# Kernel optimization log

Hardware: AMD Instinct MI355X
Metric: run time of the kernel (lower is better)

Reference implementation:

```python
import jax, jax.numpy as jnp
import numpy as np

# ---- layer config (yolov3, layer_no=2) ----
STRIDE = 8
N_CLASSES = 80
IGNORE_TH = 0.7
ANCHORS_PX = np.array([[10,13],[16,30],[33,23],[30,61],[62,45],[59,119],[116,90],[156,198],[373,326]], np.float32)
ALL_ANCHORS = ANCHORS_PX / STRIDE          # [9,2] in grid units
ANCHOR_ID_LO, ANCHOR_ID_HI = 0, 2          # anchor_mask[2] = [0,1,2]
ANCHORS = ALL_ANCHORS[ANCHOR_ID_LO:ANCHOR_ID_HI+1]  # [3,2]
NA = 3
NC = N_CLASSES + 5

B, IN_CH, NG, NBOX = 16, 256, 76, 50


def _safe_log(p):
    # emulate torch BCE's log clamp at -100; eps stops 0*inf -> nan
    return jnp.maximum(jnp.log(jnp.maximum(p, 1e-12)), -100.0)


def _bce_sum(p, t, w=None):
    l = -(t * _safe_log(p) + (1.0 - t) * _safe_log(1.0 - p))
    if w is not None:
        l = l * w
    return l.sum()


def setup_inputs() -> dict:
    key = jax.random.key(0)
    k1, k2, k3, k4, k5 = jax.random.split(key, 5)
    xin = jax.random.normal(k1, (B, IN_CH, NG, NG), jnp.float32)
    cls = jax.random.randint(k2, (B, NBOX, 1), 0, N_CLASSES).astype(jnp.float32)
    cxy = jax.random.uniform(k3, (B, NBOX, 2), jnp.float32, 0.02, 0.98)
    wh = jax.random.uniform(k4, (B, NBOX, 2), jnp.float32, 0.02, 0.40)
    labels = jnp.concatenate([cls, cxy, wh], axis=-1)  # [B,N,5]
    W = jax.random.normal(k5, (NA * NC, IN_CH), jnp.float32) * 0.02  # 1x1 conv
    b = jnp.zeros((NA * NC,), jnp.float32)
    return {"xin": xin, "labels": labels, "W": W, "b": b}


def _yolo_loss(xin, labels, W, b):
    nB, _, nG, _ = xin.shape
    anchors = jnp.asarray(ANCHORS, xin.dtype)          # [3,2]
    all_anchors = jnp.asarray(ALL_ANCHORS, xin.dtype)  # [9,2]

    # 1x1 conv -> [B, A, G, G, C]
    x = jnp.einsum('bchw,oc->bohw', xin, W) + b[None, :, None, None]
    x = x.reshape(nB, NA, NC, nG, nG).transpose(0, 1, 3, 4, 2)

    xy = jax.nn.sigmoid(x[..., :2])
    wh = x[..., 2:4]
    conf_cls = jax.nn.sigmoid(x[..., 4:])  # [B,A,G,G,1+ncls]

    gy, gx = jnp.meshgrid(jnp.arange(nG, dtype=x.dtype), jnp.arange(nG, dtype=x.dtype), indexing='ij')
    pred_boxes = jnp.stack([
        xy[..., 0] + gx,
        xy[..., 1] + gy,
        jnp.exp(wh[..., 0]) * anchors[:, 0][None, :, None, None],
        jnp.exp(wh[..., 1]) * anchors[:, 1][None, :, None, None]], axis=-1)  # [B,A,G,G,4]

    # ---- ground truth ----
    valid = labels.sum(-1) > 0                     # [B,N]
    gt_cls = labels[..., 0].astype(jnp.int32)
    gt = labels[..., 1:] * nG                      # [B,N,4] cx,cy,w,h in grid units
    gt_x, gt_y, gt_w, gt_h = gt[..., 0], gt[..., 1], gt[..., 2], gt[..., 3]
    gi = jnp.floor(gt_x).astype(jnp.int32)
    gj = jnp.floor(gt_y).astype(jnp.int32)

    # best anchor per gt: wh-IoU vs all 9 anchors (centered at origin)
    inter_a = jnp.minimum(gt_w[..., None], all_anchors[:, 0]) * jnp.minimum(gt_h[..., None], all_anchors[:, 1])
    union_a = gt_w[..., None] * gt_h[..., None] + all_anchors[:, 0] * all_anchors[:, 1] - inter_a
    best = jnp.argmax(inter_a / union_a, axis=-1)  # [B,N]
    in_mask = (best >= ANCHOR_ID_LO) & (best <= ANCHOR_ID_HI)
    a = jnp.where(in_mask, best % 3, -1)           # [B,N]

    # all-pairs IoU: pred boxes vs gt boxes (ignore mask)
    pb = pred_boxes.reshape(nB, -1, 4)             # [B,M,4], M = A*G*G
    pa_area = pb[..., 2] * pb[..., 3]
    gt_area = gt_w * gt_h
    tl = jnp.maximum(pb[:, :, None, :2] - pb[:, :, None, 2:] / 2, gt[:, None, :, :2] - gt[:, None, :, 2:] / 2)
    br = jnp.minimum(pb[:, :, None, :2] + pb[:, :, None, 2:] / 2, gt[:, None, :, :2] + gt[:, None, :, 2:] / 2)
    inter = jnp.prod(br - tl, -1) * jnp.all(tl < br, -1)
    iou = inter / (pa_area[:, :, None] + gt_area[:, None, :] - inter)
    iou = jnp.where(valid[:, None, :], iou, 0.0)
    best_iou = iou.max(-1)                         # [B,M]
    has_boxes = valid.any(-1)
    obj_mask = jnp.where(has_boxes[:, None], best_iou <= IGNORE_TH, True).reshape(nB, NA, nG, nG)

    # ---- scatter target assignment ----
    assign = valid & (a >= 0)
    a_safe = jnp.clip(a, 0, NA - 1)
    aw = anchors[a_safe, 0]
    ah = anchors[a_safe, 1]
    tvec = jnp.concatenate([
        (gt_x - jnp.floor(gt_x))[..., None],
        (gt_y - jnp.floor(gt_y))[..., None],
        jnp.log(gt_w / aw + 1e-16)[..., None],
        jnp.log(gt_h / ah + 1e-16)[..., None],
        jnp.ones_like(gt_x)[..., None],
        jax.nn.one_hot(gt_cls, N_CLASSES, dtype=x.dtype)], axis=-1)  # [B,N,NC]
    sval = 2.0 - gt_w * gt_h / (nG * nG)

    bf = jnp.broadcast_to(jnp.arange(nB)[:, None], a.shape).reshape(-1)
    af = jnp.where(assign, a_safe, NA).reshape(-1)  # NA is OOB -> dropped
    jf = gj.reshape(-1)
    if_ = gi.reshape(-1)

    target = jnp.zeros((nB, NA, nG, nG, NC), x.dtype).at[bf, af, jf, if_].set(tvec.reshape(-1, NC), mode='drop')
    scale = jnp.zeros((nB, NA, nG, nG), x.dtype).at[bf, af, jf, if_].set(sval.reshape(-1), mode='drop')
    obj_mask = obj_mask.at[bf, af, jf, if_].set(True, mode='drop')
    noobj = jnp.zeros((nB, NA, nG, nG), bool).at[bf, af, jf, if_].set(True, mode='drop')

    # ---- losses ----
    nm = noobj.astype(x.dtype)[..., None]
    p_obj = conf_cls[..., 0] * obj_mask
    t_obj = target[..., 4] * obj_mask
    p_xy = xy * nm
    t_xy = target[..., :2] * nm
    p_wh = wh * nm
    t_wh = target[..., 2:4] * nm
    p_cls = conf_cls[..., 1:] * nm
    t_cls = target[..., 5:] * nm
    sc = scale[..., None]

    loss_xy = _bce_sum(p_xy, t_xy, sc)
    rs = jnp.sqrt(sc)
    loss_wh = 0.5 * jnp.sum((p_wh * rs - t_wh * rs) ** 2)
    loss_obj = _bce_sum(p_obj, t_obj)
    loss_cls = _bce_sum(p_cls, t_cls)
    loss = loss_xy + loss_wh + loss_obj + loss_cls
    return jnp.stack([loss, loss_xy, loss_wh, loss_obj, loss_cls])


def reference(xin, labels, W, b):
    return _yolo_loss(xin, labels, W, b)
```

## Files before the change

kernel.cpp:

```cpp
#include <hip/hip_runtime.h>
#include <math.h>

#define NB    16
#define NAg   3
#define NCg   85
#define NCLS  80
#define NGg   76
#define NSp   (NGg*NGg)
#define NCELL (NAg*NSp)
#define NBOX  50
#define INCH  256

#define ACC_OFF  0
#define WIN_OFF  32
#define GD_OFF   (WIN_OFF + NB*NCELL*4)
#define GI_OFF   (GD_OFF + NB*NBOX*10*4)
#define PART_OFF (GI_OFF + NB*NBOX*2*4)
#define PART_SZ1 ((size_t)NB*15*NSp*4)
#define NEED4    (PART_OFF + 4*PART_SZ1)
#define NEED1    (PART_OFF + 1*PART_SZ1)
#define ZERO_BYTES GD_OFF

__device__ __constant__ float c_AW[9] = {1.25f,2.0f,4.125f,3.75f,7.75f,7.375f,14.5f,19.5f,46.625f};
__device__ __constant__ float c_AH[9] = {1.625f,3.75f,2.875f,7.625f,5.625f,14.875f,11.25f,24.75f,40.75f};

__device__ __forceinline__ float safe_log(float p) {
    return fmaxf(logf(fmaxf(p, 1e-12f)), -100.0f);
}
__device__ __forceinline__ float sigm(float x) {
    return 1.0f / (1.0f + expf(-x));
}

template<int NSLICE>
__global__ __launch_bounds__(256) void k_gemm_part(
    const float* __restrict__ xin, const float* __restrict__ W,
    float* __restrict__ part)
{
    constexpr int CPS = INCH / NSLICE;
    const int g  = blockIdx.x * 256 + threadIdx.x;
    if (g >= NSp/4) return;
    const int b  = blockIdx.y;
    const int sl = blockIdx.z;
    const int s0 = g * 4;

    float4 acc[15];
#pragma unroll
    for (int f = 0; f < 15; f++) acc[f] = make_float4(0.f,0.f,0.f,0.f);

    const float* xp = xin + ((size_t)b * INCH + sl * CPS) * NSp + s0;
    const float* wp = W + sl * CPS;
#pragma unroll 8
    for (int c = 0; c < CPS; c++) {
        const float4 v = *(const float4*)(xp + (size_t)c * NSp);
#pragma unroll
        for (int f = 0; f < 15; f++) {
            const int row = (f / 5) * NCg + (f % 5);
            const float w = wp[row * INCH + c];
            acc[f].x += w * v.x; acc[f].y += w * v.y;
            acc[f].z += w * v.z; acc[f].w += w * v.w;
        }
    }
#pragma unroll
    for (int f = 0; f < 15; f++)
        *(float4*)&part[(((size_t)sl * NB + b) * 15 + f) * NSp + s0] = acc[f];
}

__global__ void k_labels(const float* __restrict__ labels,
                         float* __restrict__ gdata, int* __restrict__ gint,
                         int* __restrict__ win)
{
    int t = blockIdx.x * blockDim.x + threadIdx.x;
    if (t >= NB * NBOX) return;
    int b = t / NBOX, n = t % NBOX;

    const float* L = labels + (size_t)t * 5;
    float l0 = L[0], l1 = L[1], l2 = L[2], l3 = L[3], l4 = L[4];
    int valid = (l0 + l1 + l2 + l3 + l4) > 0.f;

    float gx = l1 * NGg, gy = l2 * NGg, gw = l3 * NGg, gh = l4 * NGg;

    int best = 0; float brr = -1.f;
#pragma unroll
    for (int k = 0; k < 9; k++) {
        float inter = fminf(gw, c_AW[k]) * fminf(gh, c_AH[k]);
        float uni   = gw*gh + c_AW[k]*c_AH[k] - inter;
        float r     = inter / uni;
        if (r > brr) { brr = r; best = k; }
    }
    int a = (best <= 2) ? best : -1;
    int assign = valid && (a >= 0);
    int a_safe = a < 0 ? 0 : (a > 2 ? 2 : a);

    float* gd = gdata + (size_t)t * 10;
    gd[0] = gx; gd[1] = gy; gd[2] = gw; gd[3] = gh;
    gd[4] = gx - floorf(gx);
    gd[5] = gy - floorf(gy);
    gd[6] = logf(gw / c_AW[a_safe] + 1e-16f);
    gd[7] = logf(gh / c_AH[a_safe] + 1e-16f);
    gd[8] = 2.f - gw * gh / (float)NSp;
    gd[9] = valid ? 1.f : 0.f;

    int gi = (int)floorf(gx), gj = (int)floorf(gy);
    int inb = (gi >= 0) && (gi < NGg) && (gj >= 0) && (gj < NGg);
    int cell = (assign && inb) ? (a * NSp + gj * NGg + gi) : -1;
    gint[t*2 + 0] = cell;
    gint[t*2 + 1] = (int)l0;

    if (cell >= 0) atomicMax(&win[b * NCELL + cell], n + 1);
}

template<int NSLICE>
__global__ __launch_bounds__(256) void k_fuse(
    const float* __restrict__ part, const float* __restrict__ bias,
    const float* __restrict__ gdata, const int* __restrict__ win,
    float* __restrict__ acc)
{
    __shared__ float sb[NBOX][5];
    __shared__ int sHas;
    __shared__ float red[256];

    const int b = blockIdx.y;
    const int tid = threadIdx.x;

    if (tid < NBOX) {
        const float* gd = gdata + ((size_t)b * NBOX + tid) * 10;
        sb[tid][0] = gd[0]; sb[tid][1] = gd[1];
        sb[tid][2] = gd[2]; sb[tid][3] = gd[3];
        sb[tid][4] = gd[9];
    }
    if (tid == 0) sHas = 0;
    __syncthreads();
    if (tid < NBOX && sb[tid][4] > 0.f) atomicOr(&sHas, 1);
    __syncthreads();

    const int cell = blockIdx.x * 256 + tid;
    float l = 0.f;
    if (cell < NCELL) {
        const int a = cell / NSp, s = cell % NSp;
        float x0 = 0.f, x1 = 0.f, x2 = 0.f, x3 = 0.f, x4 = 0.f;
#pragma unroll
        for (int sl = 0; sl < NSLICE; sl++) {
            const float* pp = part + (((size_t)sl * NB + b) * 15 + a * 5) * NSp + s;
            x0 += pp[0*NSp]; x1 += pp[1*NSp]; x2 += pp[2*NSp];
            x3 += pp[3*NSp]; x4 += pp[4*NSp];
        }
        const float gxf = (float)(s % NGg);
        const float gyf = (float)(s / NGg);
        float px = sigm(x0 + bias[a*NCg+0]) + gxf;
        float py = sigm(x1 + bias[a*NCg+1]) + gyf;
        float pw = expf(x2 + bias[a*NCg+2]) * c_AW[a];
        float ph = expf(x3 + bias[a*NCg+3]) * c_AH[a];
        float cf = sigm(x4 + bias[a*NCg+4]);
        float pa = pw * ph;
        float bi = 0.f;
        for (int n = 0; n < NBOX; n++) {
            if (sb[n][4] > 0.f) {
                float gx = sb[n][0], gy = sb[n][1], gw = sb[n][2], gh = sb[n][3];
                float tlx = fmaxf(px - pw*0.5f, gx - gw*0.5f);
                float tly = fmaxf(py - ph*0.5f, gy - gh*0.5f);
                float brx = fminf(px + pw*0.5f, gx + gw*0.5f);
                float bry = fminf(py + ph*0.5f, gy + gh*0.5f);
                float inter = ((tlx < brx) && (tly < bry)) ? (brx-tlx)*(bry-tly) : 0.f;
                float iou = inter / (pa + gw*gh - inter);
                bi = fmaxf(bi, iou);
            }
        }
        bool maskpre  = sHas ? (bi <= 0.7f) : true;
        bool assigned = win[b * NCELL + cell] > 0;
        if (maskpre || assigned) {
            float t = assigned ? 1.f : 0.f;
            l = -(t * safe_log(cf) + (1.f - t) * safe_log(1.f - cf));
        }
    }
    red[tid] = l;
    __syncthreads();
    for (int o = 128; o > 0; o >>= 1) {
        if (tid < o) red[tid] += red[tid + o];
        __syncthreads();
    }
    if (tid == 0) atomicAdd(&acc[2], red[0]);
}

__global__ __launch_bounds__(256) void k_assigned(
    const float* __restrict__ xin, const float* __restrict__ W,
    const float* __restrict__ bias, const float* __restrict__ gdata,
    const int* __restrict__ gint, const int* __restrict__ win,
    float* __restrict__ acc)
{
    const int t = blockIdx.x;
    const int b = t / NBOX, n = t % NBOX;
    const int cell = gint[t*2];
    if (cell < 0) return;
    if (win[b * NCELL + cell] != n + 1) return;

    const int a = cell / NSp, s = cell % NSp;
    const int o0 = a * NCg;
    const int tid = threadIdx.x;

    __shared__ float4 col4[64];
    __shared__ float  xsh[NCg];
    __shared__ float  sacc[3];

    ((float*)col4)[tid] = xin[((size_t)b * INCH + tid) * NSp + s];
    if (tid < 3) sacc[tid] = 0.f;
    __syncthreads();

    const int wid = tid >> 6, lane = tid & 63;
    for (int o = wid; o < NCg; o += 4) {
        const float4 wv = *(const float4*)&W[(size_t)(o0 + o) * INCH + lane * 4];
        const float4 cv = col4[lane];
        float p = wv.x*cv.x + wv.y*cv.y + wv.z*cv.z + wv.w*cv.w;
        for (int off = 32; off; off >>= 1) p += __shfl_down(p, off);
        if (lane == 0) xsh[o] = p + bias[o0 + o];
    }
    __syncthreads();

    if (tid < NCg) {
        const float* gd = gdata + (size_t)t * 10;
        const float sval = gd[8];
        const int gcls = gint[t*2 + 1];
        float val = xsh[tid];
        float term; int slot;
        if (tid < 2) {
            float tgt = gd[4 + tid];
            float p = sigm(val);
            term = -(tgt * safe_log(p) + (1.f - tgt) * safe_log(1.f - p)) * sval;
            slot = 0;
        } else if (tid < 4) {
            float tgt = gd[4 + tid];
            float d = val - tgt;
            term = 0.5f * sval * d * d;
            slot = 1;
        } else if (tid == 4) {
            term = 0.f; slot = 2;
        } else {
            float tgt = ((tid - 5) == gcls) ? 1.f : 0.f;
            float p = sigm(val);
            term = -(tgt * safe_log(p) + (1.f - tgt) * safe_log(1.f - p));
            slot = 2;
        }
        atomicAdd(&sacc[slot], term);
    }
    __syncthreads();
    if (tid == 0) {
        atomicAdd(&acc[0], sacc[0]);
        atomicAdd(&acc[1], sacc[1]);
        atomicAdd(&acc[3], sacc[2]);
    }
}

__global__ void k_final(const float* __restrict__ acc, float* __restrict__ out)
{
    float xy = acc[0], wh = acc[1], ob = acc[2], cl = acc[3];
    out[0] = xy + wh + ob + cl;
    out[1] = xy; out[2] = wh; out[3] = ob; out[4] = cl;
}

extern "C" void kernel_launch(void* const* d_in, const int* in_sizes, int n_in,
                              void* d_out, int out_size, void* d_ws, size_t ws_size,
                              hipStream_t stream)
{
    const float* xin    = (const float*)d_in[0];
    const float* labels = (const float*)d_in[1];
    const float* W      = (const float*)d_in[2];
    const float* bias   = (const float*)d_in[3];

    char* ws = (char*)d_ws;
    float* acc   = (float*)(ws + ACC_OFF);
    int*   win   = (int*)  (ws + WIN_OFF);
    float* gdata = (float*)(ws + GD_OFF);
    int*   gint  = (int*)  (ws + GI_OFF);
    float* part  = (float*)(ws + PART_OFF);
    float* out   = (float*)d_out;

    const bool big = (ws_size >= (size_t)NEED4);

    hipMemsetAsync(ws, 0, ZERO_BYTES, stream);

    k_labels<<<dim3((NB*NBOX + 255)/256), 256, 0, stream>>>(labels, gdata, gint, win);

    const int gx = (NSp/4 + 255) / 256;
    if (big) k_gemm_part<4><<<dim3(gx, NB, 4), 256, 0, stream>>>(xin, W, part);
    else     k_gemm_part<1><<<dim3(gx, NB, 1), 256, 0, stream>>>(xin, W, part);

    const int fx = (NCELL + 255) / 256;
    if (big) k_fuse<4><<<dim3(fx, NB), 256, 0, stream>>>(part, bias, gdata, win, acc);
    else     k_fuse<1><<<dim3(fx, NB), 256, 0, stream>>>(part, bias, gdata, win, acc);

    k_assigned<<<dim3(NB*NBOX), 256, 0, stream>>>(xin, W, bias, gdata, gint, win, acc);
    k_final<<<1, 1, 0, stream>>>(acc, out);
}
```

Before: 203.3 us.

## Fuse partial 1x1-conv GEMM with objectness loss using in-block channel split

```diff
diff --git a/kernel.cpp b/kernel.cpp
--- a/kernel.cpp
+++ b/kernel.cpp
@@ -7,22 +7,21 @@
 #define NCLS  80
 #define NGg   76
 #define NSp   (NGg*NGg)
+#define NG4   (NSp/4)
 #define NCELL (NAg*NSp)
 #define NBOX  50
 #define INCH  256
+#define NTILE 23
 
 #define ACC_OFF  0
 #define WIN_OFF  32
 #define GD_OFF   (WIN_OFF + NB*NCELL*4)
 #define GI_OFF   (GD_OFF + NB*NBOX*10*4)
-#define PART_OFF (GI_OFF + NB*NBOX*2*4)
-#define PART_SZ1 ((size_t)NB*15*NSp*4)
-#define NEED4    (PART_OFF + 4*PART_SZ1)
-#define NEED1    (PART_OFF + 1*PART_SZ1)
 #define ZERO_BYTES GD_OFF
 
 __device__ __constant__ float c_AW[9] = {1.25f,2.0f,4.125f,3.75f,7.75f,7.375f,14.5f,19.5f,46.625f};
 __device__ __constant__ float c_AH[9] = {1.625f,3.75f,2.875f,7.625f,5.625f,14.875f,11.25f,24.75f,40.75f};
+__device__ __constant__ int   c_ROW[15] = {0,1,2,3,4, 85,86,87,88,89, 170,171,172,173,174};
 
 __device__ __forceinline__ float safe_log(float p) {
     return fmaxf(logf(fmaxf(p, 1e-12f)), -100.0f);
@@ -31,38 +30,118 @@
     return 1.0f / (1.0f + expf(-x));
 }
 
-template<int NSLICE>
-__global__ __launch_bounds__(256) void k_gemm_part(
+__global__ __launch_bounds__(256) void k_gemm_obj(
     const float* __restrict__ xin, const float* __restrict__ W,
-    float* __restrict__ part)
-{
-    constexpr int CPS = INCH / NSLICE;
-    const int g  = blockIdx.x * 256 + threadIdx.x;
-    if (g >= NSp/4) return;
-    const int b  = blockIdx.y;
-    const int sl = blockIdx.z;
-    const int s0 = g * 4;
+    const float* __restrict__ bias, const float* __restrict__ gdata,
+    const int* __restrict__ win, float* __restrict__ acc_g)
+{
+    __shared__ float wl[15][256];
+    __shared__ float part[15][256];
+    __shared__ float sb[NBOX][5];
+    __shared__ float red[256];
+    __shared__ int   sHas;
+
+    const int tid  = threadIdx.x;
+    const int tile = blockIdx.x;
+    const int b    = blockIdx.y;
+
+#pragma unroll
+    for (int f = 0; f < 15; f++) {
+        wl[f][tid]   = W[(size_t)c_ROW[f] * INCH + tid];
+        part[f][tid] = 0.f;
+    }
+    if (tid < NBOX) {
+        const float* gd = gdata + ((size_t)b * NBOX + tid) * 10;
+        sb[tid][0] = gd[0]; sb[tid][1] = gd[1];
+        sb[tid][2] = gd[2]; sb[tid][3] = gd[3];
+        sb[tid][4] = gd[9];
+    }
+    if (tid == 0) sHas = 0;
+    __syncthreads();
+    if (tid < NBOX && sb[tid][4] > 0.f) atomicOr(&sHas, 1);
+
+    const int w    = tid >> 6, lane = tid & 63;
+    const int g    = tile * 64 + lane;
+    const int gcl  = (g < NG4) ? g : (NG4 - 1);
+    const int s0   = gcl * 4;
 
     float4 acc[15];
 #pragma unroll
     for (int f = 0; f < 15; f++) acc[f] = make_float4(0.f,0.f,0.f,0.f);
 
-    const float* xp = xin + ((size_t)b * INCH + sl * CPS) * NSp + s0;
-    const float* wp = W + sl * CPS;
-#pragma unroll 8
-    for (int c = 0; c < CPS; c++) {
-        const float4 v = *(const float4*)(xp + (size_t)c * NSp);
+    const float* xp = xin + ((size_t)b * INCH + w * 64) * NSp + s0;
+#pragma unroll 2
+    for (int c4 = 0; c4 < 16; c4++) {
+        float4 xv0 = *(const float4*)(xp + (size_t)(c4*4+0) * NSp);
+        float4 xv1 = *(const float4*)(xp + (size_t)(c4*4+1) * NSp);
+        float4 xv2 = *(const float4*)(xp + (size_t)(c4*4+2) * NSp);
+        float4 xv3 = *(const float4*)(xp + (size_t)(c4*4+3) * NSp);
 #pragma unroll
         for (int f = 0; f < 15; f++) {
-            const int row = (f / 5) * NCg + (f % 5);
-            const float w = wp[row * INCH + c];
-            acc[f].x += w * v.x; acc[f].y += w * v.y;
-            acc[f].z += w * v.z; acc[f].w += w * v.w;
+            const float4 wv = *(const float4*)&wl[f][w*64 + c4*4];
+            acc[f].x += wv.x*xv0.x + wv.y*xv1.x + wv.z*xv2.x + wv.w*xv3.x;
+            acc[f].y += wv.x*xv0.y + wv.y*xv1.y + wv.z*xv2.y + wv.w*xv3.y;
+            acc[f].z += wv.x*xv0.z + wv.y*xv1.z + wv.z*xv2.z + wv.w*xv3.z;
+            acc[f].w += wv.x*xv0.w + wv.y*xv1.w + wv.z*xv2.w + wv.w*xv3.w;
         }
     }
-#pragma unroll
-    for (int f = 0; f < 15; f++)
-        *(float4*)&part[(((size_t)sl * NB + b) * 15 + f) * NSp + s0] = acc[f];
+    __syncthreads();
+
+#pragma unroll
+    for (int f = 0; f < 15; f++) {
+        atomicAdd(&part[f][lane*4+0], acc[f].x);
+        atomicAdd(&part[f][lane*4+1], acc[f].y);
+        atomicAdd(&part[f][lane*4+2], acc[f].z);
+        atomicAdd(&part[f][lane*4+3], acc[f].w);
+    }
+    __syncthreads();
+
+    const int s = tile * 256 + tid;
+    float l = 0.f;
+    if (s < NSp) {
+        const float gxf = (float)(s % NGg);
+        const float gyf = (float)(s / NGg);
+        const int hasb = sHas;
+#pragma unroll
+        for (int a = 0; a < 3; a++) {
+            float x0 = part[a*5+0][tid] + bias[a*NCg+0];
+            float x1 = part[a*5+1][tid] + bias[a*NCg+1];
+            float x2 = part[a*5+2][tid] + bias[a*NCg+2];
+            float x3 = part[a*5+3][tid] + bias[a*NCg+3];
+            float x4 = part[a*5+4][tid] + bias[a*NCg+4];
+            float px = sigm(x0) + gxf;
+            float py = sigm(x1) + gyf;
+            float pw = expf(x2) * c_AW[a];
+            float ph = expf(x3) * c_AH[a];
+            float cf = sigm(x4);
+            float pa = pw * ph;
+            float bi = 0.f;
+            for (int n = 0; n < NBOX; n++) {
+                float gx = sb[n][0], gy = sb[n][1], gw = sb[n][2], gh = sb[n][3];
+                float tlx = fmaxf(px - pw*0.5f, gx - gw*0.5f);
+                float tly = fmaxf(py - ph*0.5f, gy - gh*0.5f);
+                float brx = fminf(px + pw*0.5f, gx + gw*0.5f);
+                float bry = fminf(py + ph*0.5f, gy + gh*0.5f);
+                float inter = ((tlx < brx) && (tly < bry)) ? (brx-tlx)*(bry-tly) : 0.f;
+                float iou = inter / (pa + gw*gh - inter);
+                iou = (sb[n][4] > 0.f) ? iou : 0.f;
+                bi = fmaxf(bi, iou);
+            }
+            bool maskpre  = hasb ? (bi <= 0.7f) : true;
+            bool assigned = win[(size_t)b * NCELL + a * NSp + s] > 0;
+            if (maskpre || assigned) {
+                float t = assigned ? 1.f : 0.f;
+                l += -(t * safe_log(cf) + (1.f - t) * safe_log(1.f - cf));
+            }
+        }
+    }
+    red[tid] = l;
+    __syncthreads();
+    for (int o = 128; o > 0; o >>= 1) {
+        if (tid < o) red[tid] += red[tid + o];
+        __syncthreads();
+    }
+    if (tid == 0) atomicAdd(&acc_g[2], red[0]);
 }
 
 __global__ void k_labels(const float* __restrict__ labels,
@@ -107,78 +186,6 @@
     gint[t*2 + 1] = (int)l0;
 
     if (cell >= 0) atomicMax(&win[b * NCELL + cell], n + 1);
-}
-
-template<int NSLICE>
-__global__ __launch_bounds__(256) void k_fuse(
-    const float* __restrict__ part, const float* __restrict__ bias,
-    const float* __restrict__ gdata, const int* __restrict__ win,
-    float* __restrict__ acc)
-{
-    __shared__ float sb[NBOX][5];
-    __shared__ int sHas;
-    __shared__ float red[256];
-
-    const int b = blockIdx.y;
-    const int tid = threadIdx.x;
-
-    if (tid < NBOX) {
-        const float* gd = gdata + ((size_t)b * NBOX + tid) * 10;
-        sb[tid][0] = gd[0]; sb[tid][1] = gd[1];
-        sb[tid][2] = gd[2]; sb[tid][3] = gd[3];
-        sb[tid][4] = gd[9];
-    }
-    if (tid == 0) sHas = 0;
-    __syncthreads();
-    if (tid < NBOX && sb[tid][4] > 0.f) atomicOr(&sHas, 1);
-    __syncthreads();
-
-    const int cell = blockIdx.x * 256 + tid;
-    float l = 0.f;
-    if (cell < NCELL) {
-        const int a = cell / NSp, s = cell % NSp;
-        float x0 = 0.f, x1 = 0.f, x2 = 0.f, x3 = 0.f, x4 = 0.f;
-#pragma unroll
-        for (int sl = 0; sl < NSLICE; sl++) {
-            const float* pp = part + (((size_t)sl * NB + b) * 15 + a * 5) * NSp + s;
-            x0 += pp[0*NSp]; x1 += pp[1*NSp]; x2 += pp[2*NSp];
-            x3 += pp[3*NSp]; x4 += pp[4*NSp];
-        }
-        const float gxf = (float)(s % NGg);
-        const float gyf = (float)(s / NGg);
-        float px = sigm(x0 + bias[a*NCg+0]) + gxf;
-        float py = sigm(x1 + bias[a*NCg+1]) + gyf;
-        float pw = expf(x2 + bias[a*NCg+2]) * c_AW[a];
-        float ph = expf(x3 + bias[a*NCg+3]) * c_AH[a];
-        float cf = sigm(x4 + bias[a*NCg+4]);
-        float pa = pw * ph;
-        float bi = 0.f;
-        for (int n = 0; n < NBOX; n++) {
-            if (sb[n][4] > 0.f) {
-                float gx = sb[n][0], gy = sb[n][1], gw = sb[n][2], gh = sb[n][3];
-                float tlx = fmaxf(px - pw*0.5f, gx - gw*0.5f);
-                float tly = fmaxf(py - ph*0.5f, gy - gh*0.5f);
-                float brx = fminf(px + pw*0.5f, gx + gw*0.5f);
-                float bry = fminf(py + ph*0.5f, gy + gh*0.5f);
-                float inter = ((tlx < brx) && (tly < bry)) ? (brx-tlx)*(bry-tly) : 0.f;
-                float iou = inter / (pa + gw*gh - inter);
-                bi = fmaxf(bi, iou);
-            }
-        }
-        bool maskpre  = sHas ? (bi <= 0.7f) : true;
-        bool assigned = win[b * NCELL + cell] > 0;
-        if (maskpre || assigned) {
-            float t = assigned ? 1.f : 0.f;
-            l = -(t * safe_log(cf) + (1.f - t) * safe_log(1.f - cf));
-        }
-    }
-    red[tid] = l;
-    __syncthreads();
-    for (int o = 128; o > 0; o >>= 1) {
-        if (tid < o) red[tid] += red[tid + o];
-        __syncthreads();
-    }
-    if (tid == 0) atomicAdd(&acc[2], red[0]);
 }
 
 __global__ __launch_bounds__(256) void k_assigned(
@@ -270,23 +277,12 @@
     int*   win   = (int*)  (ws + WIN_OFF);
     float* gdata = (float*)(ws + GD_OFF);
     int*   gint  = (int*)  (ws + GI_OFF);
-    float* part  = (float*)(ws + PART_OFF);
     float* out   = (float*)d_out;
 
-    const bool big = (ws_size >= (size_t)NEED4);
-
     hipMemsetAsync(ws, 0, ZERO_BYTES, stream);
 
-    k_labels<<<dim3((NB*NBOX + 255)/256), 256, 0, stream>>>(labels, gdata, gint, win);
-
-    const int gx = (NSp/4 + 255) / 256;
-    if (big) k_gemm_part<4><<<dim3(gx, NB, 4), 256, 0, stream>>>(xin, W, part);
-    else     k_gemm_part<1><<<dim3(gx, NB, 1), 256, 0, stream>>>(xin, W, part);
-
-    const int fx = (NCELL + 255) / 256;
-    if (big) k_fuse<4><<<dim3(fx, NB), 256, 0, stream>>>(part, bias, gdata, win, acc);
-    else     k_fuse<1><<<dim3(fx, NB), 256, 0, stream>>>(part, bias, gdata, win, acc);
-
+    k_labels  <<<dim3((NB*NBOX + 255)/256), 256, 0, stream>>>(labels, gdata, gint, win);
+    k_gemm_obj<<<dim3(NTILE, NB), 256, 0, stream>>>(xin, W, bias, gdata, win, acc);
     k_assigned<<<dim3(NB*NBOX), 256, 0, stream>>>(xin, W, bias, gdata, gint, win, acc);
-    k_final<<<1, 1, 0, stream>>>(acc, out);
-}
+    k_final   <<<1, 1, 0, stream>>>(acc, out);
+}
```

Result: slower. 235.3 us (+15.8%).
